# Kernel tuning notes

Measured on AMD Instinct MI355X. Metric: run time of the kernel, lower is better.

The kernel has to match this reference:

```python
import jax, jax.numpy as jnp
import numpy as np

NUM_EXPERTS = 32
TOP_K = 4
ALPHA = 1.702   # GPT-OSS GLU alpha
LIMIT = 7.0     # GPT-OSS clamp limit


def setup_inputs() -> dict:
    key = jax.random.key(0)
    ks = jax.random.split(key, 7)
    B, S, H, E = 2, 2048, 1024, NUM_EXPERTS
    return {
        "hidden_states": jax.random.normal(ks[0], (B, S, H), jnp.float32),
        "router_weight": jax.random.normal(ks[1], (E, H), jnp.float32) * 0.02,
        "router_bias": jax.random.normal(ks[2], (E,), jnp.float32) * 0.02,
        "gate_up_proj": jax.random.normal(ks[3], (E, H, 2 * H), jnp.float32) * 0.02,
        "gate_up_proj_bias": jax.random.normal(ks[4], (E, 2 * H), jnp.float32) * 0.02,
        "down_proj": jax.random.normal(ks[5], (E, H, H), jnp.float32) * 0.02,
        "down_proj_bias": jax.random.normal(ks[6], (E, H), jnp.float32) * 0.02,
    }


def _moe_forward(hidden_states, router_weight, router_bias,
                 gate_up_proj, gate_up_proj_bias, down_proj, down_proj_bias):
    B, S, H = hidden_states.shape
    E, K = NUM_EXPERTS, TOP_K
    T = B * S
    capacity = T * K // E * 2  # expert_capacity as in the torch module

    x = hidden_states.reshape(T, H)

    # ---- router: linear -> top-k -> softmax over top-k -> dense scatter ----
    logits = x @ router_weight.T + router_bias                     # [T, E]
    top_vals, top_idx = jax.lax.top_k(logits, K)                   # [T, K]
    weights = jax.nn.softmax(top_vals, axis=-1)                    # [T, K]
    router_scores = jnp.zeros_like(logits).at[
        jnp.arange(T)[:, None], top_idx].set(weights)              # [T, E]

    # ---- capacity-based dispatch (first-come-first-served in token order) ----
    flat_e = top_idx.reshape(-1)                                   # [T*K]
    token_id = jnp.repeat(jnp.arange(T), K)                        # [T*K]
    onehot = (flat_e[:, None] == jnp.arange(E)[None, :]).astype(jnp.int32)
    # rank of each assignment within its expert (0-based, arrival order)
    rank = jnp.take_along_axis(jnp.cumsum(onehot, axis=0),
                               flat_e[:, None], axis=1)[:, 0] - 1  # [T*K]
    valid = rank < capacity
    slot = jnp.where(valid, rank, capacity)  # out-of-range slot -> dropped

    buffer = jnp.zeros((E, capacity, H), x.dtype).at[flat_e, slot].set(
        x[token_id], mode="drop")                                  # [E, C, H]

    # ---- grouped expert MLP: gate_up GEMM + GPT-OSS GLU + down GEMM ----
    gu = jnp.einsum("ech,ehf->ecf", buffer, gate_up_proj) \
         + gate_up_proj_bias[:, None, :]                           # [E, C, 2H]
    gate = gu[..., ::2]
    up = gu[..., 1::2]
    gate = jnp.minimum(gate, LIMIT)
    up = jnp.clip(up, -LIMIT, LIMIT)
    glu = gate * jax.nn.sigmoid(gate * ALPHA)
    act = (up + 1.0) * glu                                         # [E, C, H]
    expert_out = jnp.einsum("ech,ehf->ecf", act, down_proj) \
                 + down_proj_bias[:, None, :]                      # [E, C, H]

    # ---- weighted combine (dropped tokens contribute zero) ----
    gathered = expert_out[flat_e, jnp.where(valid, rank, 0)]       # [T*K, H]
    w = router_scores[token_id, flat_e] * valid.astype(x.dtype)    # [T*K]
    out = jax.ops.segment_sum(gathered * w[:, None], token_id,
                              num_segments=T)                      # [T, H]
    return out.reshape(B, S, H), router_scores


def reference(hidden_states, router_weight, router_bias, gate_up_proj,
              gate_up_proj_bias, down_proj, down_proj_bias):
    return _moe_forward(hidden_states, router_weight, router_bias,
                        gate_up_proj, gate_up_proj_bias, down_proj,
                        down_proj_bias)
```

## Files before the change

### kernel.cpp

```cpp
#include <hip/hip_runtime.h>
#include <hip/hip_bf16.h>

#define T_TOK 4096
#define H_DIM 1024
#define E_EXP 32
#define TOPK 4
#define CAP 1024
#define PAIRS (T_TOK*TOPK)

typedef __attribute__((ext_vector_type(8))) short short8v;
typedef __attribute__((ext_vector_type(4))) float f32x4;
typedef unsigned long long u64;
typedef unsigned short ushort;

__device__ __forceinline__ float bf16_bits_to_f32(ushort h) {
    return __uint_as_float(((unsigned)h) << 16);
}
__device__ __forceinline__ unsigned bf16r(float f) {
    unsigned u = __float_as_uint(f);
    return ((u + 0x7fffu + ((u >> 16) & 1u)) >> 16) & 0xffffu;
}
__device__ __forceinline__ unsigned cvt2(float a, float b) {
    unsigned r;
    asm("v_cvt_pk_bf16_f32 %0, %1, %2" : "=v"(r) : "v"(a), "v"(b));
    return r;
}
__device__ __forceinline__ u64 pk4(float a, float b, float c, float d) {
    return (u64)cvt2(a, b) | ((u64)cvt2(c, d) << 32);
}

#define GLD16(gsrc, ldst) \
    __builtin_amdgcn_global_load_lds( \
        (const __attribute__((address_space(1))) unsigned*)(gsrc), \
        (__attribute__((address_space(3))) unsigned*)(ldst), 16, 0, 0)

#define WAIT_VM(N)   asm volatile("s_waitcnt vmcnt(" #N ")" ::: "memory")
#define WAIT_VMLG(N) asm volatile("s_waitcnt vmcnt(" #N ") lgkmcnt(0)" ::: "memory")
#define WAIT_LG()    asm volatile("s_waitcnt lgkmcnt(0)" ::: "memory")
#define SCHEDB()     __builtin_amdgcn_sched_barrier(0)
#define BARRIER()    __builtin_amdgcn_s_barrier()

__global__ void zero_kernel(float4* __restrict__ p, int n4) {
    int i = blockIdx.x * blockDim.x + threadIdx.x;
    if (i < n4) p[i] = make_float4(0.f, 0.f, 0.f, 0.f);
}

__global__ __launch_bounds__(256) void router_kernel(
    const float* __restrict__ x, const float* __restrict__ rw,
    const float* __restrict__ rb, float* __restrict__ scores,
    int* __restrict__ flat_e, float* __restrict__ flat_w)
{
    __shared__ float xs[8][H_DIM];
    __shared__ float lg[8][E_EXP];
    const int t0 = blockIdx.x * 8;
    const int tid = threadIdx.x;

    for (int i = tid; i < 2048; i += 256) {
        int row = i >> 8, c4 = i & 255;
        *(float4*)&xs[row][c4 * 4] =
            *(const float4*)(x + (size_t)(t0 + row) * H_DIM + c4 * 4);
    }
    __syncthreads();

    const int e = tid >> 3, l8 = tid & 7;
    float part[8];
    #pragma unroll
    for (int tt = 0; tt < 8; ++tt) part[tt] = 0.f;
    const float* wrow = rw + (size_t)e * H_DIM;
    for (int h = l8; h < H_DIM; h += 8) {
        float w = wrow[h];
        #pragma unroll
        for (int tt = 0; tt < 8; ++tt) part[tt] = fmaf(xs[tt][h], w, part[tt]);
    }
    #pragma unroll
    for (int tt = 0; tt < 8; ++tt) {
        float v = part[tt];
        v += __shfl_xor(v, 1);
        v += __shfl_xor(v, 2);
        v += __shfl_xor(v, 4);
        if (l8 == 0) lg[tt][e] = v + rb[e];
    }
    __syncthreads();

    if (tid < 8) {
        const int tt = tid, t = t0 + tt;
        unsigned used = 0;
        float bv[TOPK]; int bi[TOPK];
        #pragma unroll
        for (int j = 0; j < TOPK; j++) {
            float best = -1e30f; int bid = -1;
            for (int q = 0; q < E_EXP; q++) {
                if (used & (1u << q)) continue;
                if (lg[tt][q] > best) { best = lg[tt][q]; bid = q; }
            }
            used |= 1u << bid;
            bv[j] = best; bi[j] = bid;
        }
        const float m = bv[0];
        float s = 0.f; float w[TOPK];
        #pragma unroll
        for (int j = 0; j < TOPK; j++) { w[j] = expf(bv[j] - m); s += w[j]; }
        const float inv = 1.f / s;
        #pragma unroll
        for (int j = 0; j < TOPK; j++) w[j] *= inv;
        for (int q = 0; q < E_EXP; ++q) {
            float v = 0.f;
            #pragma unroll
            for (int j = 0; j < TOPK; j++) if (bi[j] == q) v = w[j];
            scores[(size_t)t * E_EXP + q] = v;
        }
        #pragma unroll
        for (int j = 0; j < TOPK; j++) {
            flat_e[t * TOPK + j] = bi[j];
            flat_w[t * TOPK + j] = w[j];
        }
    }
}

__global__ __launch_bounds__(256) void scan_kernel(
    const int* __restrict__ flat_e, const float* __restrict__ flat_w,
    int* __restrict__ slot_token, float* __restrict__ slot_w,
    int* __restrict__ counts)
{
    __shared__ int cnt[256 * E_EXP];
    const int tid = threadIdx.x;
    for (int e = 0; e < E_EXP; e++) cnt[tid * E_EXP + e] = 0;
    __syncthreads();
    const int base = tid * (PAIRS / 256);
    for (int i = 0; i < PAIRS / 256; i++) {
        int e = flat_e[base + i];
        cnt[tid * E_EXP + e]++;
    }
    __syncthreads();
    if (tid < E_EXP) {
        int run = 0;
        for (int i = 0; i < 256; i++) {
            int idx = i * E_EXP + tid;
            int v = cnt[idx];
            cnt[idx] = run;
            run += v;
        }
        counts[tid] = min(run, CAP);
    }
    __syncthreads();
    for (int i = 0; i < PAIRS / 256; i++) {
        int p = base + i;
        int e = flat_e[p];
        int r = cnt[tid * E_EXP + e]++;
        if (r < CAP) {
            slot_token[e * CAP + r] = p >> 2;
            slot_w[e * CAP + r] = flat_w[p];
        }
    }
}

__global__ __launch_bounds__(256) void stage_tokens(
    const float* __restrict__ x, const int* __restrict__ slot_token,
    const int* __restrict__ counts, char* __restrict__ xbuf)
{
    const int e = blockIdx.y, rt = blockIdx.x;
    const int n = counts[e];
    const int row0 = rt * 128;
    if (row0 >= n) return;
    const int rows_here = min(128, n - row0);
    const int lane = threadIdx.x & 63, wv = threadIdx.x >> 6;
    char* tb = xbuf + ((size_t)(e * 8 + rt)) * 262144;

    for (int r = wv; r < rows_here; r += 4) {
        const float* xr = x + (size_t)slot_token[e * CAP + row0 + r] * H_DIM;
        const int s = (r >> 1) & 3;
        #pragma unroll
        for (int half = 0; half < 2; ++half) {
            int gi = half * 64 + lane;
            float4 a = *(const float4*)(xr + gi * 8);
            float4 b = *(const float4*)(xr + gi * 8 + 4);
            uint4 w;
            w.x = cvt2(a.x, a.y); w.y = cvt2(a.z, a.w);
            w.z = cvt2(b.x, b.y); w.w = cvt2(b.z, b.w);
            int t = gi >> 2, kq = gi & 3;
            *(uint4*)(tb + (size_t)t * 8192 + r * 64 + ((kq ^ s) * 16)) = w;
        }
    }
}

__global__ __launch_bounds__(256, 3) void gateup_mfma(
    const char* __restrict__ xbuf, const float* __restrict__ wgu,
    const float* __restrict__ gub, const int* __restrict__ counts,
    char* __restrict__ act)
{
    const int lin = blockIdx.x;
    const int xcd = lin & 7, slot = lin >> 3;
    const int gg = (slot >> 3) * 8 + xcd;
    const int rt = slot & 7;
    const int e = gg >> 4, ct = gg & 15;

    const int n = counts[e];
    const int row0 = rt * 128;
    if (row0 >= n) return;
    const int rows_here = min(128, n - row0);
    const int c0f = ct * 64, c0gu = ct * 128;

    __shared__ char AsB[3][8192];
    __shared__ char BgB[2][4096];
    __shared__ char BuB[2][4096];

    const int tid = threadIdx.x;
    const int lane = tid & 63, wid = tid >> 6;
    const int wr = wid >> 1, wc = wid & 1;
    const int l15 = lane & 15, l4 = lane >> 4;
    const int kq = tid >> 5;
    const int p2 = tid & 31;

    const char* xtile = xbuf + ((size_t)(e * 8 + rt)) * 262144;

    f32x4 accg[4][2], accu[4][2];
    #pragma unroll
    for (int m = 0; m < 4; m++)
        #pragma unroll
        for (int j = 0; j < 2; j++) { accg[m][j] = (f32x4)0.f; accu[m][j] = (f32x4)0.f; }

    float4 bv0[4], bv1[4], bv2[4];

#define GU_STAGE_A(BUF, T) { \
    const char* sa_ = xtile + (size_t)(T) * 8192 + tid * 16; \
    GLD16(sa_, AsB[BUF] + tid * 16); \
    GLD16(sa_ + 4096, AsB[BUF] + 4096 + tid * 16); }

#define GU_BLOAD(BV, T) { \
    const float* sb_ = wgu + ((size_t)e * 1024 + (T) * 32 + kq * 4) * 2048 + c0gu + 4 * p2; \
    BV[0] = *(const float4*)(sb_); \
    BV[1] = *(const float4*)(sb_ + 2048); \
    BV[2] = *(const float4*)(sb_ + 4096); \
    BV[3] = *(const float4*)(sb_ + 6144); }

#define GU_BPACK(BUF, BV) { \
    char* dg_ = BgB[BUF] + (kq >> 1) * 1024 + (2 * p2) * 16 + (kq & 1) * 8; \
    char* du_ = BuB[BUF] + (kq >> 1) * 1024 + (2 * p2) * 16 + (kq & 1) * 8; \
    *(u64*)dg_        = pk4(BV[0].x, BV[1].x, BV[2].x, BV[3].x); \
    *(u64*)(dg_ + 16) = pk4(BV[0].z, BV[1].z, BV[2].z, BV[3].z); \
    *(u64*)du_        = pk4(BV[0].y, BV[1].y, BV[2].y, BV[3].y); \
    *(u64*)(du_ + 16) = pk4(BV[0].w, BV[1].w, BV[2].w, BV[3].w); }

#define GU_COMPUTE(AC, BC) { \
    short8v afr[4]; \
    _Pragma("unroll") \
    for (int m = 0; m < 4; ++m) { \
        int row_ = wr * 64 + m * 16 + l15; \
        afr[m] = *(short8v*)(AsB[AC] + row_ * 64 + ((l4 ^ ((row_ >> 1) & 3)) * 16)); \
    } \
    __builtin_amdgcn_s_setprio(1); \
    _Pragma("unroll") \
    for (int j = 0; j < 2; ++j) { \
        int fl_ = wc * 32 + j * 16 + l15; \
        short8v bg8 = *(short8v*)(BgB[BC] + l4 * 1024 + fl_ * 16); \
        short8v bu8 = *(short8v*)(BuB[BC] + l4 * 1024 + fl_ * 16); \
        _Pragma("unroll") \
        for (int m = 0; m < 4; ++m) { \
            accg[m][j] = __builtin_amdgcn_mfma_f32_16x16x32_bf16(afr[m], bg8, accg[m][j], 0, 0, 0); \
            accu[m][j] = __builtin_amdgcn_mfma_f32_16x16x32_bf16(afr[m], bu8, accu[m][j], 0, 0, 0); \
        } \
    } \
    __builtin_amdgcn_s_setprio(0); }

    GU_STAGE_A(0, 0);
    GU_BLOAD(bv0, 0);
    GU_BLOAD(bv1, 1);
    GU_STAGE_A(1, 1);
    GU_BLOAD(bv2, 2);
    WAIT_VM(10); SCHEDB();
    GU_BPACK(0, bv0);
    WAIT_LG(); SCHEDB();
    BARRIER(); SCHEDB();

#define GU_IT(T, A2, LS, PS, AC, BC, BN) { \
    GU_STAGE_A(A2, (T) + 2); \
    GU_BLOAD(bv##LS, (T) + 3); \
    GU_COMPUTE(AC, BC); SCHEDB(); \
    WAIT_VM(12); SCHEDB(); \
    GU_BPACK(BN, bv##PS); \
    WAIT_VMLG(10); SCHEDB(); \
    BARRIER(); SCHEDB(); }

    for (int t6 = 0; t6 < 24; t6 += 6) {
        GU_IT(t6 + 0, 2, 0, 1, 0, 0, 1)
        GU_IT(t6 + 1, 0, 1, 2, 1, 1, 0)
        GU_IT(t6 + 2, 1, 2, 0, 2, 0, 1)
        GU_IT(t6 + 3, 2, 0, 1, 0, 1, 0)
        GU_IT(t6 + 4, 0, 1, 2, 1, 0, 1)
        GU_IT(t6 + 5, 1, 2, 0, 2, 1, 0)
    }
    GU_IT(24, 2, 0, 1, 0, 0, 1)
    GU_IT(25, 0, 1, 2, 1, 1, 0)
    GU_IT(26, 1, 2, 0, 2, 0, 1)
    GU_IT(27, 2, 0, 1, 0, 1, 0)
    GU_IT(28, 0, 1, 2, 1, 0, 1)
    GU_STAGE_A(1, 31);
    GU_COMPUTE(2, 1); SCHEDB();
    WAIT_VM(8); SCHEDB();
    GU_BPACK(0, bv0);
    WAIT_VMLG(6); SCHEDB();
    BARRIER(); SCHEDB();
    GU_COMPUTE(0, 0); SCHEDB();
    WAIT_VM(2); SCHEDB();
    GU_BPACK(1, bv1);
    WAIT_VMLG(0); SCHEDB();
    BARRIER(); SCHEDB();
    GU_COMPUTE(1, 1);

#undef GU_IT
#undef GU_COMPUTE
#undef GU_BPACK
#undef GU_BLOAD
#undef GU_STAGE_A

    char* atile = act + ((size_t)(e * 8 + rt)) * 262144;
    #pragma unroll
    for (int j = 0; j < 2; ++j) {
        int f = c0f + wc * 32 + j * 16 + l15;
        float bgb = gub[(size_t)e * 2048 + 2 * f];
        float bub = gub[(size_t)e * 2048 + 2 * f + 1];
        int tt = f >> 5, kq2 = (f & 31) >> 3, ke = f & 7;
        #pragma unroll
        for (int m = 0; m < 4; ++m) {
            int rbase = wr * 64 + m * 16 + l4 * 4;
            #pragma unroll
            for (int reg = 0; reg < 4; ++reg) {
                int r = rbase + reg;
                if (r >= rows_here) continue;
                float g = accg[m][j][reg] + bgb;
                float u = accu[m][j][reg] + bub;
                g = fminf(g, 7.0f);
                u = fminf(fmaxf(u, -7.0f), 7.0f);
                float glu = g / (1.0f + __expf(-1.702f * g));
                float a = (u + 1.0f) * glu;
                *(ushort*)(atile + (size_t)tt * 8192 + r * 64 +
                           ((kq2 ^ ((r >> 1) & 3)) * 16) + ke * 2) = (ushort)bf16r(a);
            }
        }
    }
}

__global__ __launch_bounds__(256, 3) void down_mfma(
    const char* __restrict__ act, const float* __restrict__ wd,
    const float* __restrict__ db, const int* __restrict__ counts,
    const int* __restrict__ slot_token, const float* __restrict__ slot_w,
    float* __restrict__ out)
{
    const int lin = blockIdx.x;
    const int xcd = lin & 7, slot = lin >> 3;
    const int gg = (slot >> 3) * 8 + xcd;
    const int rt = slot & 7;
    const int e = gg >> 3, ct = gg & 7;

    const int n = counts[e];
    const int row0 = rt * 128;
    if (row0 >= n) return;
    const int rows_here = min(128, n - row0);
    const int c0 = ct * 128;

    __shared__ char AsB[3][8192];
    __shared__ char BsB[2][8192];
    __shared__ int tok_s[128];
    __shared__ float wrow_s[128];

    const int tid = threadIdx.x;
    if (tid < 128) {
        if (tid < rows_here) {
            tok_s[tid] = slot_token[e * CAP + row0 + tid];
            wrow_s[tid] = slot_w[e * CAP + row0 + tid];
        } else { tok_s[tid] = 0; wrow_s[tid] = 0.f; }
    }
    __syncthreads();

    const int lane = tid & 63, wid = tid >> 6;
    const int wr = wid >> 1, wc = wid & 1;
    const int l15 = lane & 15, l4 = lane >> 4;
    const int kq = tid >> 5;
    const int p2 = tid & 31;

    const char* atile = act + ((size_t)(e * 8 + rt)) * 262144;

    f32x4 acc[4][4];
    #pragma unroll
    for (int m = 0; m < 4; m++)
        #pragma unroll
        for (int j = 0; j < 4; j++) acc[m][j] = (f32x4)0.f;

    float4 bv0[4], bv1[4], bv2[4];

#define DN_STAGE_A(BUF, T) { \
    const char* sa_ = atile + (size_t)(T) * 8192 + tid * 16; \
    GLD16(sa_, AsB[BUF] + tid * 16); \
    GLD16(sa_ + 4096, AsB[BUF] + 4096 + tid * 16); }

#define DN_BLOAD(BV, T) { \
    const float* sb_ = wd + ((size_t)e * 1024 + (T) * 32 + kq * 4) * 1024 + c0 + 4 * p2; \
    BV[0] = *(const float4*)(sb_); \
    BV[1] = *(const float4*)(sb_ + 1024); \
    BV[2] = *(const float4*)(sb_ + 2048); \
    BV[3] = *(const float4*)(sb_ + 3072); }

#define DN_BPACK(BUF, BV) { \
    char* d0_ = BsB[BUF] + (kq >> 1) * 2048 + (4 * p2) * 16 + (kq & 1) * 8; \
    *(u64*)d0_        = pk4(BV[0].x, BV[1].x, BV[2].x, BV[3].x); \
    *(u64*)(d0_ + 16) = pk4(BV[0].y, BV[1].y, BV[2].y, BV[3].y); \
    *(u64*)(d0_ + 32) = pk4(BV[0].z, BV[1].z, BV[2].z, BV[3].z); \
    *(u64*)(d0_ + 48) = pk4(BV[0].w, BV[1].w, BV[2].w, BV[3].w); }

#define DN_COMPUTE(AC, BC) { \
    short8v afr[4]; \
    _Pragma("unroll") \
    for (int m = 0; m < 4; ++m) { \
        int row_ = wr * 64 + m * 16 + l15; \
        afr[m] = *(short8v*)(AsB[AC] + row_ * 64 + ((l4 ^ ((row_ >> 1) & 3)) * 16)); \
    } \
    __builtin_amdgcn_s_setprio(1); \
    _Pragma("unroll") \
    for (int j = 0; j < 4; ++j) { \
        int nn_ = wc * 64 + j * 16 + l15; \
        short8v b8 = *(short8v*)(BsB[BC] + l4 * 2048 + nn_ * 16); \
        _Pragma("unroll") \
        for (int m = 0; m < 4; ++m) \
            acc[m][j] = __builtin_amdgcn_mfma_f32_16x16x32_bf16(afr[m], b8, acc[m][j], 0, 0, 0); \
    } \
    __builtin_amdgcn_s_setprio(0); }

    DN_STAGE_A(0, 0);
    DN_BLOAD(bv0, 0);
    DN_BLOAD(bv1, 1);
    DN_STAGE_A(1, 1);
    DN_BLOAD(bv2, 2);
    WAIT_VM(10); SCHEDB();
    DN_BPACK(0, bv0);
    WAIT_LG(); SCHEDB();
    BARRIER(); SCHEDB();

#define DN_IT(T, A2, LS, PS, AC, BC, BN) { \
    DN_STAGE_A(A2, (T) + 2); \
    DN_BLOAD(bv##LS, (T) + 3); \
    DN_COMPUTE(AC, BC); SCHEDB(); \
    WAIT_VM(12); SCHEDB(); \
    DN_BPACK(BN, bv##PS); \
    WAIT_VMLG(10); SCHEDB(); \
    BARRIER(); SCHEDB(); }

    for (int t6 = 0; t6 < 24; t6 += 6) {
        DN_IT(t6 + 0, 2, 0, 1, 0, 0, 1)
        DN_IT(t6 + 1, 0, 1, 2, 1, 1, 0)
        DN_IT(t6 + 2, 1, 2, 0, 2, 0, 1)
        DN_IT(t6 + 3, 2, 0, 1, 0, 1, 0)
        DN_IT(t6 + 4, 0, 1, 2, 1, 0, 1)
        DN_IT(t6 + 5, 1, 2, 0, 2, 1, 0)
    }
    DN_IT(24, 2, 0, 1, 0, 0, 1)
    DN_IT(25, 0, 1, 2, 1, 1, 0)
    DN_IT(26, 1, 2, 0, 2, 0, 1)
    DN_IT(27, 2, 0, 1, 0, 1, 0)
    DN_IT(28, 0, 1, 2, 1, 0, 1)
    DN_STAGE_A(1, 31);
    DN_COMPUTE(2, 1); SCHEDB();
    WAIT_VM(8); SCHEDB();
    DN_BPACK(0, bv0);
    WAIT_VMLG(6); SCHEDB();
    BARRIER(); SCHEDB();
    DN_COMPUTE(0, 0); SCHEDB();
    WAIT_VM(2); SCHEDB();
    DN_BPACK(1, bv1);
    WAIT_VMLG(0); SCHEDB();
    BARRIER(); SCHEDB();
    DN_COMPUTE(1, 1);

#undef DN_IT
#undef DN_COMPUTE
#undef DN_BPACK
#undef DN_BLOAD
#undef DN_STAGE_A

    #pragma unroll
    for (int j = 0; j < 4; ++j) {
        int col = c0 + wc * 64 + j * 16 + l15;
        float bias = db[(size_t)e * H_DIM + col];
        #pragma unroll
        for (int m = 0; m < 4; ++m) {
            int rbase = wr * 64 + m * 16 + l4 * 4;
            #pragma unroll
            for (int reg = 0; reg < 4; ++reg) {
                int r = rbase + reg;
                if (r >= rows_here) continue;
                atomicAdd(out + (size_t)tok_s[r] * H_DIM + col,
                          wrow_s[r] * (acc[m][j][reg] + bias));
            }
        }
    }
}

extern "C" void kernel_launch(void* const* d_in, const int* in_sizes, int n_in,
                              void* d_out, int out_size, void* d_ws, size_t ws_size,
                              hipStream_t stream) {
    const float* x   = (const float*)d_in[0];
    const float* rw  = (const float*)d_in[1];
    const float* rb  = (const float*)d_in[2];
    const float* wgu = (const float*)d_in[3];
    const float* gub = (const float*)d_in[4];
    const float* wd  = (const float*)d_in[5];
    const float* db  = (const float*)d_in[6];

    float* out    = (float*)d_out;
    float* scores = out + (size_t)T_TOK * H_DIM;

    char* ws = (char*)d_ws;
    char* xbuf = ws;
    size_t off = (size_t)E_EXP * CAP * H_DIM * 2;
    char* act  = ws + off;  off += (size_t)E_EXP * CAP * H_DIM * 2;
    int*   flat_e     = (int*)(ws + off);   off += PAIRS * 4;
    float* flat_w     = (float*)(ws + off); off += PAIRS * 4;
    int*   slot_token = (int*)(ws + off);   off += E_EXP * CAP * 4;
    float* slot_w     = (float*)(ws + off); off += E_EXP * CAP * 4;
    int*   counts     = (int*)(ws + off);   off += E_EXP * 4;
    (void)ws_size; (void)out_size; (void)n_in; (void)in_sizes;

    hipLaunchKernelGGL(zero_kernel, dim3(4096), dim3(256), 0, stream,
                       (float4*)out, (T_TOK * H_DIM) / 4);
    hipLaunchKernelGGL(router_kernel, dim3(T_TOK / 8), dim3(256), 0, stream,
                       x, rw, rb, scores, flat_e, flat_w);
    hipLaunchKernelGGL(scan_kernel, dim3(1), dim3(256), 0, stream,
                       flat_e, flat_w, slot_token, slot_w, counts);
    hipLaunchKernelGGL(stage_tokens, dim3(8, E_EXP), dim3(256), 0, stream,
                       x, slot_token, counts, xbuf);
    hipLaunchKernelGGL(gateup_mfma, dim3(4096), dim3(256), 0, stream,
                       xbuf, wgu, gub, counts, act);
    hipLaunchKernelGGL(down_mfma, dim3(2048), dim3(256), 0, stream,
                       act, wd, db, counts, slot_token, slot_w, out);
}
```

Measured before the change: 452.5 us.

## Replace atomic scatter-combine with bf16 expert output buffer and gather finalize kernel

```diff
diff --git a/kernel.cpp b/kernel.cpp
--- a/kernel.cpp
+++ b/kernel.cpp
@@ -39,11 +39,6 @@
 #define WAIT_LG()    asm volatile("s_waitcnt lgkmcnt(0)" ::: "memory")
 #define SCHEDB()     __builtin_amdgcn_sched_barrier(0)
 #define BARRIER()    __builtin_amdgcn_s_barrier()
-
-__global__ void zero_kernel(float4* __restrict__ p, int n4) {
-    int i = blockIdx.x * blockDim.x + threadIdx.x;
-    if (i < n4) p[i] = make_float4(0.f, 0.f, 0.f, 0.f);
-}
 
 __global__ __launch_bounds__(256) void router_kernel(
     const float* __restrict__ x, const float* __restrict__ rw,
@@ -120,7 +115,7 @@
 __global__ __launch_bounds__(256) void scan_kernel(
     const int* __restrict__ flat_e, const float* __restrict__ flat_w,
     int* __restrict__ slot_token, float* __restrict__ slot_w,
-    int* __restrict__ counts)
+    int* __restrict__ pair_slot, int* __restrict__ counts)
 {
     __shared__ int cnt[256 * E_EXP];
     const int tid = threadIdx.x;
@@ -150,6 +145,9 @@
         if (r < CAP) {
             slot_token[e * CAP + r] = p >> 2;
             slot_w[e * CAP + r] = flat_w[p];
+            pair_slot[p] = r;
+        } else {
+            pair_slot[p] = -1;
         }
     }
 }
@@ -343,8 +341,7 @@
 __global__ __launch_bounds__(256, 3) void down_mfma(
     const char* __restrict__ act, const float* __restrict__ wd,
     const float* __restrict__ db, const int* __restrict__ counts,
-    const int* __restrict__ slot_token, const float* __restrict__ slot_w,
-    float* __restrict__ out)
+    ushort* __restrict__ eout)
 {
     const int lin = blockIdx.x;
     const int xcd = lin & 7, slot = lin >> 3;
@@ -360,18 +357,8 @@
 
     __shared__ char AsB[3][8192];
     __shared__ char BsB[2][8192];
-    __shared__ int tok_s[128];
-    __shared__ float wrow_s[128];
 
     const int tid = threadIdx.x;
-    if (tid < 128) {
-        if (tid < rows_here) {
-            tok_s[tid] = slot_token[e * CAP + row0 + tid];
-            wrow_s[tid] = slot_w[e * CAP + row0 + tid];
-        } else { tok_s[tid] = 0; wrow_s[tid] = 0.f; }
-    }
-    __syncthreads();
-
     const int lane = tid & 63, wid = tid >> 6;
     const int wr = wid >> 1, wc = wid & 1;
     const int l15 = lane & 15, l4 = lane >> 4;
@@ -487,11 +474,36 @@
             for (int reg = 0; reg < 4; ++reg) {
                 int r = rbase + reg;
                 if (r >= rows_here) continue;
-                atomicAdd(out + (size_t)tok_s[r] * H_DIM + col,
-                          wrow_s[r] * (acc[m][j][reg] + bias));
+                eout[((size_t)e * CAP + row0 + r) * H_DIM + col] =
+                    (ushort)bf16r(acc[m][j][reg] + bias);
             }
         }
     }
+}
+
+__global__ __launch_bounds__(256) void finalize_kernel(
+    const ushort* __restrict__ eout, const int* __restrict__ flat_e,
+    const float* __restrict__ flat_w, const int* __restrict__ pair_slot,
+    float* __restrict__ out)
+{
+    const int t = blockIdx.x;
+    const int c = threadIdx.x * 4;
+    float a0 = 0.f, a1 = 0.f, a2 = 0.f, a3 = 0.f;
+    #pragma unroll
+    for (int k = 0; k < TOPK; ++k) {
+        int p = t * TOPK + k;
+        int s = pair_slot[p];
+        if (s < 0) continue;
+        int e = flat_e[p];
+        float w = flat_w[p];
+        const ushort* row = eout + ((size_t)e * CAP + s) * H_DIM + c;
+        ushort4 v = *(const ushort4*)row;
+        a0 += w * bf16_bits_to_f32(v.x);
+        a1 += w * bf16_bits_to_f32(v.y);
+        a2 += w * bf16_bits_to_f32(v.z);
+        a3 += w * bf16_bits_to_f32(v.w);
+    }
+    *(float4*)(out + (size_t)t * H_DIM + c) = make_float4(a0, a1, a2, a3);
 }
 
 extern "C" void kernel_launch(void* const* d_in, const int* in_sizes, int n_in,
@@ -511,24 +523,26 @@
     char* ws = (char*)d_ws;
     char* xbuf = ws;
     size_t off = (size_t)E_EXP * CAP * H_DIM * 2;
-    char* act  = ws + off;  off += (size_t)E_EXP * CAP * H_DIM * 2;
+    char* act  = ws + off;    off += (size_t)E_EXP * CAP * H_DIM * 2;
+    ushort* eout = (ushort*)(ws + off); off += (size_t)E_EXP * CAP * H_DIM * 2;
     int*   flat_e     = (int*)(ws + off);   off += PAIRS * 4;
     float* flat_w     = (float*)(ws + off); off += PAIRS * 4;
     int*   slot_token = (int*)(ws + off);   off += E_EXP * CAP * 4;
     float* slot_w     = (float*)(ws + off); off += E_EXP * CAP * 4;
+    int*   pair_slot  = (int*)(ws + off);   off += PAIRS * 4;
     int*   counts     = (int*)(ws + off);   off += E_EXP * 4;
-    (void)ws_size; (void)out_size; (void)n_in; (void)in_sizes;
-
-    hipLaunchKernelGGL(zero_kernel, dim3(4096), dim3(256), 0, stream,
-                       (float4*)out, (T_TOK * H_DIM) / 4);
+    (void)ws_size; (void)out_size; (void)n_in; (void)in_sizes; (void)slot_w;
+
     hipLaunchKernelGGL(router_kernel, dim3(T_TOK / 8), dim3(256), 0, stream,
                        x, rw, rb, scores, flat_e, flat_w);
     hipLaunchKernelGGL(scan_kernel, dim3(1), dim3(256), 0, stream,
-                       flat_e, flat_w, slot_token, slot_w, counts);
+                       flat_e, flat_w, slot_token, slot_w, pair_slot, counts);
     hipLaunchKernelGGL(stage_tokens, dim3(8, E_EXP), dim3(256), 0, stream,
                        x, slot_token, counts, xbuf);
     hipLaunchKernelGGL(gateup_mfma, dim3(4096), dim3(256), 0, stream,
                        xbuf, wgu, gub, counts, act);
     hipLaunchKernelGGL(down_mfma, dim3(2048), dim3(256), 0, stream,
-                       act, wd, db, counts, slot_token, slot_w, out);
-}
+                       act, wd, db, counts, eout);
+    hipLaunchKernelGGL(finalize_kernel, dim3(T_TOK), dim3(256), 0, stream,
+                       eout, flat_e, flat_w, pair_slot, out);
+}
```

New measurement: 438.7 us, median of 2. 3.1% less time.
